# Performance work log

Measured on AMD Instinct MI355X. Metric: run time of the kernel, lower is better.

## Reference

```python
import jax, jax.numpy as jnp
import numpy as np

N_HEAD = 16
MASKED_BIAS = -10000.0


def setup_inputs() -> dict:
    key = jax.random.key(0)
    k1, k2, k3 = jax.random.split(key, 3)
    B, T, E = 2, 2048, 1024
    return {
        "stacked": jax.random.normal(k1, (B, T, E), dtype=jnp.float32),
        "w_attn": jax.random.normal(k2, (E, 3 * E), dtype=jnp.float32) * 0.02,
        "b_attn": jnp.zeros((3 * E,), dtype=jnp.float32),
        "w_proj": jax.random.normal(k3, (E, E), dtype=jnp.float32) * 0.02,
        "b_proj": jnp.zeros((E,), dtype=jnp.float32),
    }


def reference(stacked, w_attn, b_attn, w_proj, b_proj):
    B, T, E = stacked.shape
    nh = N_HEAD
    dh = E // nh
    # Conv1D (GPT-2): x @ W + b
    qkv = stacked @ w_attn + b_attn            # (B, T, 3E)
    q, k, v = jnp.split(qkv, 3, axis=-1)
    q = q.reshape(B, T, nh, dh).transpose(0, 2, 1, 3)  # (B, nh, T, dh)
    k = k.reshape(B, T, nh, dh).transpose(0, 2, 1, 3)
    v = v.reshape(B, T, nh, dh).transpose(0, 2, 1, 3)
    # scores = Q @ K^T / sqrt(dh)
    w = jnp.einsum("bhtd,bhsd->bhts", q, k) / jnp.sqrt(jnp.float32(dh))
    causal = jnp.tril(jnp.ones((T, T), dtype=bool))
    w = jnp.where(causal, w, jnp.float32(MASKED_BIAS))
    w = jax.nn.softmax(w, axis=-1)
    out = jnp.einsum("bhts,bhsd->bhtd", w, v)  # (B, nh, T, dh)
    out = out.transpose(0, 2, 1, 3).reshape(B, T, E)
    attn_z = out @ w_proj + b_proj
    return attn_z
```

## Files before the change

kernel.cpp:

```cpp
#include <hip/hip_runtime.h>
#include <hip/hip_bf16.h>

#define B_ 2
#define T_ 2048
#define E_ 1024
#define NH 16
#define M_ (B_*T_)
#define N3E 3072

typedef __attribute__((ext_vector_type(8))) short short8;
typedef __attribute__((ext_vector_type(4))) float f32x4;

__device__ __forceinline__ unsigned short f2bf(float f) {
  unsigned u = __builtin_bit_cast(unsigned, f);
  unsigned r = 0x7FFFu + ((u >> 16) & 1u);
  return (unsigned short)((u + r) >> 16);
}

__device__ __forceinline__ float bf2f(unsigned short s) {
  return __builtin_bit_cast(float, ((unsigned)s) << 16);
}

__device__ __forceinline__ unsigned cvtpk(float a, float b) {
  unsigned r;
  asm("v_cvt_pk_bf16_f32 %0, %1, %2" : "=v"(r) : "v"(a), "v"(b));
  return r;
}

__device__ __forceinline__ float exp2fast(float x) {
  float r;
  asm("v_exp_f32 %0, %1" : "=v"(r) : "v"(x));
  return r;
}

__device__ __forceinline__ void gload16(const void* g, void* l) {
  __builtin_amdgcn_global_load_lds(
      (const __attribute__((address_space(1))) unsigned int*)g,
      (__attribute__((address_space(3))) unsigned int*)l, 16, 0, 0);
}

__device__ __forceinline__ f32x4 mfma16(short8 a, short8 b, f32x4 c) {
  return __builtin_amdgcn_mfma_f32_16x16x32_bf16(a, b, c, 0, 0, 0);
}

__global__ __launch_bounds__(256) void prep_kernel(
    const float* __restrict__ stacked, const float* __restrict__ w_attn,
    const float* __restrict__ w_proj, unsigned short* __restrict__ Abf,
    unsigned short* __restrict__ WaT, unsigned short* __restrict__ WpT) {
  __shared__ float tile[32][33];
  const int bx = blockIdx.x;
  const int tid = threadIdx.x;
  if (bx < 2048) {
    int i = bx * 256 + tid;
    const float4* p = (const float4*)stacked + (size_t)i * 2;
    float4 a = p[0], b = p[1];
    short8 o;
    o[0] = (short)f2bf(a.x); o[1] = (short)f2bf(a.y);
    o[2] = (short)f2bf(a.z); o[3] = (short)f2bf(a.w);
    o[4] = (short)f2bf(b.x); o[5] = (short)f2bf(b.y);
    o[6] = (short)f2bf(b.z); o[7] = (short)f2bf(b.w);
    *(short8*)(Abf + (size_t)i * 8) = o;
    return;
  }
  const float* in;
  unsigned short* out;
  int R, C, c0, r0;
  if (bx < 5120) {
    int b = bx - 2048;
    in = w_attn; out = WaT; R = E_; C = N3E;
    c0 = (b % 96) * 32; r0 = (b / 96) * 32;
  } else {
    int b = bx - 5120;
    in = w_proj; out = WpT; R = E_; C = E_;
    c0 = (b % 32) * 32; r0 = (b / 32) * 32;
  }
  int tx = tid & 31, ty = tid >> 5;
#pragma unroll
  for (int i = 0; i < 4; i++) {
    int r = ty + i * 8;
    tile[r][tx] = in[(size_t)(r0 + r) * C + c0 + tx];
  }
  __syncthreads();
#pragma unroll
  for (int i = 0; i < 4; i++) {
    int r = ty + i * 8;
    out[(size_t)(c0 + r) * R + r0 + tx] = f2bf(tile[tx][r]);
  }
}

__global__ __launch_bounds__(256) void vtrans_kernel(
    const unsigned short* __restrict__ qkv, unsigned short* __restrict__ Vt) {
  const int s0 = blockIdx.x * 64;
  const int c0 = blockIdx.y * 64;
  const int b = blockIdx.z;
  __shared__ unsigned short t[64][72];
  const int tid = threadIdx.x;
  const size_t rs = 3 * E_;
  const unsigned short* src = qkv + (size_t)(b * T_) * rs + 2 * E_;
#pragma unroll
  for (int p = 0; p < 2; p++) {
    int idx = tid + p * 256;
    int r = idx >> 3, c = (idx & 7) * 8;
    *(short8*)&t[r][c] = *(const short8*)(src + (size_t)(s0 + r) * rs + c0 + c);
  }
  __syncthreads();
#pragma unroll
  for (int p = 0; p < 2; p++) {
    int idx = tid + p * 256;
    int dr = idx >> 3, sc = (idx & 7) * 8;
    short8 o;
#pragma unroll
    for (int j = 0; j < 8; j++) o[j] = (short)t[sc + j][dr];
    *(short8*)&Vt[(size_t)(b * E_ + c0 + dr) * T_ + s0 + sc] = o;
  }
}

__global__ __launch_bounds__(512, 2) void gemm256(
    const unsigned short* __restrict__ A, const unsigned short* __restrict__ Bt,
    const float* __restrict__ bias, unsigned short* __restrict__ outp,
    int M, int N, int K) {
  __shared__ __attribute__((aligned(16))) unsigned short Asm[2][256 * 64];
  __shared__ __attribute__((aligned(16))) unsigned short Bsm[2][256 * 64];
  const int tid = threadIdx.x;
  const int lane = tid & 63, wid = tid >> 6;
  const int wr = wid >> 2, wcn = wid & 3;
  const int li = lane & 15, g = lane >> 4;
  const int sw = li & 7;

  const int ntx = N >> 8;
  const int nwg = (M >> 8) * ntx;
  const int cpx = nwg >> 3;
  const int logical = (blockIdx.x & 7) * cpx + (blockIdx.x >> 3);
  const int bm = (logical / ntx) << 8;
  const int bn = (logical % ntx) << 8;

  f32x4 acc[8][4] = {};

#pragma unroll
  for (int p = 0; p < 4; p++) {
    int idx = tid + p * 512;
    int r = idx >> 3, ch = idx & 7;
    gload16(A + (size_t)(bm + r) * K + ((ch ^ (r & 7)) << 3),
            (char*)&Asm[0][0] + idx * 16);
  }
#pragma unroll
  for (int p = 0; p < 4; p++) {
    int idx = tid + p * 512;
    int r = idx >> 3, ch = idx & 7;
    gload16(Bt + (size_t)(bn + r) * K + ((ch ^ (r & 7)) << 3),
            (char*)&Bsm[0][0] + idx * 16);
  }
  asm volatile("s_waitcnt vmcnt(0)" ::: "memory");
  __syncthreads();

  const int NT = K >> 6;
  for (int t = 0; t < NT; t++) {
    const int buf = t & 1;
    const unsigned short* As = &Asm[buf][0];
    const unsigned short* Bs = &Bsm[buf][0];
    const int kn = (t + 1) << 6;
    const bool pre = (t + 1 < NT);
#pragma unroll
    for (int q = 0; q < 4; q++) {
      const int mh = q >> 1, nh2 = q & 1;
      short8 a[4][2], bfr[2][2];
#pragma unroll
      for (int mf = 0; mf < 4; mf++) {
        const int R = wr * 128 + (mh * 4 + mf) * 16 + li;
        a[mf][0] = *(const short8*)&As[R * 64 + ((g ^ sw) << 3)];
        a[mf][1] = *(const short8*)&As[R * 64 + (((4 + g) ^ sw) << 3)];
      }
#pragma unroll
      for (int nf = 0; nf < 2; nf++) {
        const int S = wcn * 64 + (nh2 * 2 + nf) * 16 + li;
        bfr[nf][0] = *(const short8*)&Bs[S * 64 + ((g ^ sw) << 3)];
        bfr[nf][1] = *(const short8*)&Bs[S * 64 + (((4 + g) ^ sw) << 3)];
      }
      if (pre && q == 0) {
#pragma unroll
        for (int p = 0; p < 4; p++) {
          int idx = tid + p * 512;
          int r = idx >> 3, ch = idx & 7;
          gload16(A + (size_t)(bm + r) * K + kn + ((ch ^ (r & 7)) << 3),
                  (char*)&Asm[buf ^ 1][0] + idx * 16);
        }
      }
      if (pre && q == 1) {
#pragma unroll
        for (int p = 0; p < 4; p++) {
          int idx = tid + p * 512;
          int r = idx >> 3, ch = idx & 7;
          gload16(Bt + (size_t)(bn + r) * K + kn + ((ch ^ (r & 7)) << 3),
                  (char*)&Bsm[buf ^ 1][0] + idx * 16);
        }
      }
      __builtin_amdgcn_sched_barrier(0);
      __builtin_amdgcn_s_setprio(1);
#pragma unroll
      for (int mf = 0; mf < 4; mf++)
#pragma unroll
        for (int nf = 0; nf < 2; nf++) {
          f32x4 c = acc[mh * 4 + mf][nh2 * 2 + nf];
          c = mfma16(a[mf][0], bfr[nf][0], c);
          c = mfma16(a[mf][1], bfr[nf][1], c);
          acc[mh * 4 + mf][nh2 * 2 + nf] = c;
        }
      __builtin_amdgcn_s_setprio(0);
      __builtin_amdgcn_sched_barrier(0);
    }
    asm volatile("s_waitcnt vmcnt(0)" ::: "memory");
    __syncthreads();
  }

#pragma unroll
  for (int nf = 0; nf < 4; nf++) {
    int col = bn + wcn * 64 + nf * 16 + li;
    float bs = bias[col];
#pragma unroll
    for (int mf = 0; mf < 8; mf++) {
      int row0 = bm + wr * 128 + mf * 16 + g * 4;
#pragma unroll
      for (int r = 0; r < 4; r++)
        outp[(size_t)(row0 + r) * N + col] = f2bf(acc[mf][nf][r] + bs);
    }
  }
}

template <int OUTF32>
__global__ __launch_bounds__(256) void gemm_bt(
    const unsigned short* __restrict__ A, const unsigned short* __restrict__ Bt,
    const float* __restrict__ bias, void* __restrict__ outp,
    int M, int N, int K) {
  __shared__ __attribute__((aligned(16))) unsigned short Asm[2][128 * 32];
  __shared__ __attribute__((aligned(16))) unsigned short Bsm[2][128 * 32];
  const int tid = threadIdx.x;
  const int lane = tid & 63;
  const int wid = tid >> 6;
  const int wr = wid >> 1, wc = wid & 1;
  const int li = lane & 15, g = lane >> 4;

  const int ntx = N >> 7;
  const int nwg = (M >> 7) * ntx;
  const int cpx = nwg >> 3;
  const int logical = (blockIdx.x & 7) * cpx + (blockIdx.x >> 3);
  const int bm = (logical / ntx) << 7;
  const int bn = (logical % ntx) << 7;

  f32x4 acc[4][4] = {};

  const int srow = tid >> 2;
  const int scol = (tid & 3) * 8;
  const unsigned short* Ag = A + (size_t)(bm + srow) * K + scol;
  const unsigned short* Bg = Bt + (size_t)(bn + srow) * K + scol;
  const int ldsoff = tid * 16;

  gload16(Ag, (char*)&Asm[0][0] + ldsoff);
  gload16(Ag + (size_t)64 * K, (char*)&Asm[0][0] + ldsoff + 4096);
  gload16(Bg, (char*)&Bsm[0][0] + ldsoff);
  gload16(Bg + (size_t)64 * K, (char*)&Bsm[0][0] + ldsoff + 4096);
  asm volatile("s_waitcnt vmcnt(0)" ::: "memory");
  __syncthreads();

  int cur = 0;
  for (int k0 = 0; k0 < K; k0 += 32) {
    const bool pre = (k0 + 32 < K);
    if (pre) {
      const int k1 = k0 + 32;
      gload16(Ag + k1, (char*)&Asm[cur ^ 1][0] + ldsoff);
      gload16(Ag + (size_t)64 * K + k1,
              (char*)&Asm[cur ^ 1][0] + ldsoff + 4096);
      gload16(Bg + k1, (char*)&Bsm[cur ^ 1][0] + ldsoff);
      gload16(Bg + (size_t)64 * K + k1,
              (char*)&Bsm[cur ^ 1][0] + ldsoff + 4096);
    }
    short8 af[4], bf[4];
#pragma unroll
    for (int i = 0; i < 4; i++)
      af[i] = *(const short8*)&Asm[cur][(wr * 64 + i * 16 + li) * 32 + g * 8];
#pragma unroll
    for (int j = 0; j < 4; j++)
      bf[j] = *(const short8*)&Bsm[cur][(wc * 64 + j * 16 + li) * 32 + g * 8];
    __builtin_amdgcn_s_setprio(1);
#pragma unroll
    for (int i = 0; i < 4; i++)
#pragma unroll
      for (int j = 0; j < 4; j++)
        acc[i][j] = __builtin_amdgcn_mfma_f32_16x16x32_bf16(af[i], bf[j],
                                                            acc[i][j], 0, 0, 0);
    __builtin_amdgcn_s_setprio(0);
    if (pre) asm volatile("s_waitcnt vmcnt(0)" ::: "memory");
    __syncthreads();
    cur ^= 1;
  }

#pragma unroll
  for (int j = 0; j < 4; j++) {
    int col = bn + wc * 64 + j * 16 + li;
    float bs = bias[col];
#pragma unroll
    for (int i = 0; i < 4; i++) {
      int row0 = bm + wr * 64 + i * 16 + g * 4;
#pragma unroll
      for (int r = 0; r < 4; r++) {
        float v = acc[i][j][r] + bs;
        if (OUTF32)
          ((float*)outp)[(size_t)(row0 + r) * N + col] = v;
        else
          ((unsigned short*)outp)[(size_t)(row0 + r) * N + col] = f2bf(v);
      }
    }
  }
}

__device__ __forceinline__ void attn_tile(
    const unsigned short* Ksm, const unsigned short* Vts,
    unsigned short (*PsmW)[64], short8 qf0, short8 qf1,
    float& m2, float& l2, f32x4* O, int qrel, bool diag, int li, int g) {
  f32x4 S[4];
  __builtin_amdgcn_s_setprio(1);
#pragma unroll
  for (int ct = 0; ct < 4; ct++) {
    int r = ct * 16 + li;
    int sw = r & 7;
    short8 k0f = *(const short8*)&Ksm[r * 64 + ((g ^ sw) << 3)];
    short8 k1f = *(const short8*)&Ksm[r * 64 + (((g + 4) ^ sw) << 3)];
    f32x4 z = {0.f, 0.f, 0.f, 0.f};
    z = mfma16(k0f, qf0, z);
    z = mfma16(k1f, qf1, z);
    S[ct] = z;
  }
  __builtin_amdgcn_s_setprio(0);

  if (diag) {
#pragma unroll
    for (int ct = 0; ct < 4; ct++)
#pragma unroll
      for (int r = 0; r < 4; r++)
        if (ct * 16 + g * 4 + r > qrel) S[ct][r] = -30000.f;
  }

  float tmax = S[0][0];
#pragma unroll
  for (int ct = 0; ct < 4; ct++)
#pragma unroll
    for (int r = 0; r < 4; r++) tmax = fmaxf(tmax, S[ct][r]);
  tmax = fmaxf(tmax, __shfl_xor(tmax, 16));
  tmax = fmaxf(tmax, __shfl_xor(tmax, 32));

  if (__any(tmax > m2 + 11.5f)) {
    float mn = fmaxf(m2, tmax);
    float cs = exp2fast(m2 - mn);
    l2 *= cs;
#pragma unroll
    for (int c2 = 0; c2 < 4; c2++)
#pragma unroll
      for (int r = 0; r < 4; r++) O[c2][r] *= cs;
    m2 = mn;
  }

  float rsum = 0.f;
#pragma unroll
  for (int ct = 0; ct < 4; ct++) {
    float p0 = exp2fast(S[ct][0] - m2);
    float p1 = exp2fast(S[ct][1] - m2);
    float p2 = exp2fast(S[ct][2] - m2);
    float p3 = exp2fast(S[ct][3] - m2);
    rsum += (p0 + p1) + (p2 + p3);
    uint2 pk;
    pk.x = cvtpk(p0, p1);
    pk.y = cvtpk(p2, p3);
    int pc = (2 * ct + (g >> 1)) ^ (li & 7);
    *(uint2*)&PsmW[li][pc * 8 + (g & 1) * 4] = pk;
  }
  rsum += __shfl_xor(rsum, 16);
  rsum += __shfl_xor(rsum, 32);
  l2 += rsum;

  __builtin_amdgcn_s_setprio(1);
#pragma unroll
  for (int kk = 0; kk < 2; kk++) {
    short8 pf = *(const short8*)&PsmW[li][((4 * kk + g) ^ (li & 7)) * 8];
#pragma unroll
    for (int c2 = 0; c2 < 4; c2++) {
      int d = c2 * 16 + li;
      short8 vf = *(const short8*)&Vts[d * 64 + (((kk * 4 + g) ^ (li & 7)) << 3)];
      O[c2] = mfma16(vf, pf, O[c2]);
    }
  }
  __builtin_amdgcn_s_setprio(0);
}

__global__ __launch_bounds__(256) void attn_kernel(
    const unsigned short* __restrict__ qkv, const unsigned short* __restrict__ Vt,
    unsigned short* __restrict__ aout) {
  const int pair = blockIdx.x;
  const int h = blockIdx.y, b = blockIdx.z;
  const int qa = pair, qb = (T_ / 64 - 1) - pair;
  const int tid = threadIdx.x, lane = tid & 63, w = tid >> 6;
  const int li = lane & 15, g = lane >> 4;

  __shared__ __attribute__((aligned(16))) unsigned short Ksm[2][64 * 64];
  __shared__ __attribute__((aligned(16))) unsigned short Vts[2][64 * 64];
  __shared__ __attribute__((aligned(16))) unsigned short Psm[4][16][64];

  const size_t rs = 3 * E_;
  const unsigned short* base = qkv + (size_t)b * T_ * rs + h * 64;
  const unsigned short* Kg = base + E_;
  const unsigned short* Vtg = Vt + (size_t)(b * E_ + h * 64) * T_;

  const float QSC = 0.18033688f;
  short8 qfa0, qfa1, qfb0, qfb1;
  {
    const unsigned short* qrow = base + (size_t)(qa * 64 + w * 16 + li) * rs;
    short8 v0 = *(const short8*)(qrow + g * 8);
    short8 v1 = *(const short8*)(qrow + 32 + g * 8);
    qrow = base + (size_t)(qb * 64 + w * 16 + li) * rs;
    short8 v2 = *(const short8*)(qrow + g * 8);
    short8 v3 = *(const short8*)(qrow + 32 + g * 8);
#pragma unroll
    for (int j = 0; j < 8; j++) {
      qfa0[j] = (short)f2bf(bf2f((unsigned short)v0[j]) * QSC);
      qfa1[j] = (short)f2bf(bf2f((unsigned short)v1[j]) * QSC);
      qfb0[j] = (short)f2bf(bf2f((unsigned short)v2[j]) * QSC);
      qfb1[j] = (short)f2bf(bf2f((unsigned short)v3[j]) * QSC);
    }
  }

  float ma = -1e30f, la = 0.f, mb = -1e30f, lb = 0.f;
  f32x4 Oa[4] = {}, Ob[4] = {};

#pragma unroll
  for (int p = 0; p < 2; p++) {
    int idx = tid + p * 256;
    int r = idx >> 3, ch = idx & 7;
    int sc = (ch ^ (r & 7)) * 8;
    gload16(Kg + (size_t)r * rs + sc, (char*)&Ksm[0][0] + idx * 16);
    gload16(Vtg + (size_t)r * T_ + sc, (char*)&Vts[0][0] + idx * 16);
  }
  asm volatile("s_waitcnt vmcnt(0)" ::: "memory");
  __syncthreads();

  const int nt = qb + 1;
  for (int kv = 0; kv < nt; kv++) {
    const int cur = kv & 1, nxt = cur ^ 1;
    const bool pre = (kv + 1 < nt);
    if (pre) {
      const int s1 = (kv + 1) * 64;
#pragma unroll
      for (int p = 0; p < 2; p++) {
        int idx = tid + p * 256;
        int r = idx >> 3, ch = idx & 7;
        int sc = (ch ^ (r & 7)) * 8;
        gload16(Kg + (size_t)(s1 + r) * rs + sc,
                (char*)&Ksm[nxt][0] + idx * 16);
        gload16(Vtg + (size_t)r * T_ + s1 + sc,
                (char*)&Vts[nxt][0] + idx * 16);
      }
    }

    attn_tile(&Ksm[cur][0], &Vts[cur][0], Psm[w], qfb0, qfb1, mb, lb, Ob,
              qb * 64 + w * 16 + li - kv * 64, kv == qb, li, g);
    if (kv <= qa)
      attn_tile(&Ksm[cur][0], &Vts[cur][0], Psm[w], qfa0, qfa1, ma, la, Oa,
                qa * 64 + w * 16 + li - kv * 64, kv == qa, li, g);

    asm volatile("s_waitcnt vmcnt(0)" ::: "memory");
    __syncthreads();
  }

  const float inva = 1.f / la, invb = 1.f / lb;
  const int rowa = b * T_ + qa * 64 + w * 16 + li;
  const int rowb = b * T_ + qb * 64 + w * 16 + li;
#pragma unroll
  for (int c2 = 0; c2 < 4; c2++) {
    uint2 oa, ob;
    oa.x = cvtpk(Oa[c2][0] * inva, Oa[c2][1] * inva);
    oa.y = cvtpk(Oa[c2][2] * inva, Oa[c2][3] * inva);
    ob.x = cvtpk(Ob[c2][0] * invb, Ob[c2][1] * invb);
    ob.y = cvtpk(Ob[c2][2] * invb, Ob[c2][3] * invb);
    *(uint2*)&aout[(size_t)rowa * E_ + h * 64 + c2 * 16 + g * 4] = oa;
    *(uint2*)&aout[(size_t)rowb * E_ + h * 64 + c2 * 16 + g * 4] = ob;
  }
}

extern "C" void kernel_launch(void* const* d_in, const int* in_sizes, int n_in,
                              void* d_out, int out_size, void* d_ws,
                              size_t ws_size, hipStream_t stream) {
  const float* stacked = (const float*)d_in[0];
  const float* w_attn = (const float*)d_in[1];
  const float* b_attn = (const float*)d_in[2];
  const float* w_proj = (const float*)d_in[3];
  const float* b_proj = (const float*)d_in[4];
  float* out = (float*)d_out;

  unsigned short* Abf = (unsigned short*)d_ws;
  unsigned short* WaT = Abf + (size_t)M_ * E_;
  unsigned short* WpT = WaT + (size_t)N3E * E_;
  unsigned short* qkv = WpT + (size_t)E_ * E_;
  unsigned short* aout = qkv + (size_t)M_ * N3E;
  unsigned short* Vt = aout + (size_t)M_ * E_;

  prep_kernel<<<6144, 256, 0, stream>>>(stacked, w_attn, w_proj, Abf, WaT, WpT);
  gemm256<<<(M_ / 256) * (N3E / 256), 512, 0, stream>>>(Abf, WaT, b_attn, qkv,
                                                        M_, N3E, E_);
  vtrans_kernel<<<dim3(T_ / 64, E_ / 64, B_), 256, 0, stream>>>(qkv, Vt);
  attn_kernel<<<dim3(T_ / 128, NH, B_), 256, 0, stream>>>(qkv, Vt, aout);
  gemm_bt<1><<<(M_ / 128) * (E_ / 128), 256, 0, stream>>>(aout, WpT, b_proj,
                                                          out, M_, E_, E_);
}
```

Measured before the change: 118.1 us.

## Fuse V transpose into QKV GEMM epilogue and retile to 256x192

```diff
diff --git a/kernel.cpp b/kernel.cpp
--- a/kernel.cpp
+++ b/kernel.cpp
@@ -88,53 +88,26 @@
   }
 }
 
-__global__ __launch_bounds__(256) void vtrans_kernel(
-    const unsigned short* __restrict__ qkv, unsigned short* __restrict__ Vt) {
-  const int s0 = blockIdx.x * 64;
-  const int c0 = blockIdx.y * 64;
-  const int b = blockIdx.z;
-  __shared__ unsigned short t[64][72];
-  const int tid = threadIdx.x;
-  const size_t rs = 3 * E_;
-  const unsigned short* src = qkv + (size_t)(b * T_) * rs + 2 * E_;
-#pragma unroll
-  for (int p = 0; p < 2; p++) {
-    int idx = tid + p * 256;
-    int r = idx >> 3, c = (idx & 7) * 8;
-    *(short8*)&t[r][c] = *(const short8*)(src + (size_t)(s0 + r) * rs + c0 + c);
-  }
-  __syncthreads();
-#pragma unroll
-  for (int p = 0; p < 2; p++) {
-    int idx = tid + p * 256;
-    int dr = idx >> 3, sc = (idx & 7) * 8;
-    short8 o;
-#pragma unroll
-    for (int j = 0; j < 8; j++) o[j] = (short)t[sc + j][dr];
-    *(short8*)&Vt[(size_t)(b * E_ + c0 + dr) * T_ + s0 + sc] = o;
-  }
-}
-
-__global__ __launch_bounds__(512, 2) void gemm256(
+__global__ __launch_bounds__(512, 1) void gemm256(
     const unsigned short* __restrict__ A, const unsigned short* __restrict__ Bt,
-    const float* __restrict__ bias, unsigned short* __restrict__ outp,
-    int M, int N, int K) {
+    const float* __restrict__ bias, unsigned short* __restrict__ qkvout,
+    unsigned short* __restrict__ Vt, int M, int N, int K) {
   __shared__ __attribute__((aligned(16))) unsigned short Asm[2][256 * 64];
-  __shared__ __attribute__((aligned(16))) unsigned short Bsm[2][256 * 64];
+  __shared__ __attribute__((aligned(16))) unsigned short Bsm[2][192 * 64];
   const int tid = threadIdx.x;
   const int lane = tid & 63, wid = tid >> 6;
   const int wr = wid >> 2, wcn = wid & 3;
   const int li = lane & 15, g = lane >> 4;
   const int sw = li & 7;
 
-  const int ntx = N >> 8;
+  const int ntx = N / 192;
   const int nwg = (M >> 8) * ntx;
   const int cpx = nwg >> 3;
   const int logical = (blockIdx.x & 7) * cpx + (blockIdx.x >> 3);
   const int bm = (logical / ntx) << 8;
-  const int bn = (logical % ntx) << 8;
-
-  f32x4 acc[8][4] = {};
+  const int bn = (logical % ntx) * 192;
+
+  f32x4 acc[8][3] = {};
 
 #pragma unroll
   for (int p = 0; p < 4; p++) {
@@ -144,7 +117,7 @@
             (char*)&Asm[0][0] + idx * 16);
   }
 #pragma unroll
-  for (int p = 0; p < 4; p++) {
+  for (int p = 0; p < 3; p++) {
     int idx = tid + p * 512;
     int r = idx >> 3, ch = idx & 7;
     gload16(Bt + (size_t)(bn + r) * K + ((ch ^ (r & 7)) << 3),
@@ -160,23 +133,22 @@
     const unsigned short* Bs = &Bsm[buf][0];
     const int kn = (t + 1) << 6;
     const bool pre = (t + 1 < NT);
-#pragma unroll
-    for (int q = 0; q < 4; q++) {
-      const int mh = q >> 1, nh2 = q & 1;
-      short8 a[4][2], bfr[2][2];
-#pragma unroll
-      for (int mf = 0; mf < 4; mf++) {
-        const int R = wr * 128 + (mh * 4 + mf) * 16 + li;
-        a[mf][0] = *(const short8*)&As[R * 64 + ((g ^ sw) << 3)];
-        a[mf][1] = *(const short8*)&As[R * 64 + (((4 + g) ^ sw) << 3)];
-      }
-#pragma unroll
-      for (int nf = 0; nf < 2; nf++) {
-        const int S = wcn * 64 + (nh2 * 2 + nf) * 16 + li;
-        bfr[nf][0] = *(const short8*)&Bs[S * 64 + ((g ^ sw) << 3)];
-        bfr[nf][1] = *(const short8*)&Bs[S * 64 + (((4 + g) ^ sw) << 3)];
-      }
-      if (pre && q == 0) {
+    short8 a[4][2];
+#pragma unroll
+    for (int ph = 0; ph < 6; ph++) {
+      const int mh = ph / 3, nf3 = ph % 3;
+      if (nf3 == 0) {
+#pragma unroll
+        for (int mf = 0; mf < 4; mf++) {
+          const int R = wr * 128 + (mh * 4 + mf) * 16 + li;
+          a[mf][0] = *(const short8*)&As[R * 64 + ((g ^ sw) << 3)];
+          a[mf][1] = *(const short8*)&As[R * 64 + (((4 + g) ^ sw) << 3)];
+        }
+      }
+      const int S = wcn * 48 + nf3 * 16 + li;
+      short8 b0 = *(const short8*)&Bs[S * 64 + ((g ^ sw) << 3)];
+      short8 b1 = *(const short8*)&Bs[S * 64 + (((4 + g) ^ sw) << 3)];
+      if (pre && ph == 0) {
 #pragma unroll
         for (int p = 0; p < 4; p++) {
           int idx = tid + p * 512;
@@ -185,9 +157,9 @@
                   (char*)&Asm[buf ^ 1][0] + idx * 16);
         }
       }
-      if (pre && q == 1) {
-#pragma unroll
-        for (int p = 0; p < 4; p++) {
+      if (pre && ph == 1) {
+#pragma unroll
+        for (int p = 0; p < 3; p++) {
           int idx = tid + p * 512;
           int r = idx >> 3, ch = idx & 7;
           gload16(Bt + (size_t)(bn + r) * K + kn + ((ch ^ (r & 7)) << 3),
@@ -197,14 +169,12 @@
       __builtin_amdgcn_sched_barrier(0);
       __builtin_amdgcn_s_setprio(1);
 #pragma unroll
-      for (int mf = 0; mf < 4; mf++)
-#pragma unroll
-        for (int nf = 0; nf < 2; nf++) {
-          f32x4 c = acc[mh * 4 + mf][nh2 * 2 + nf];
-          c = mfma16(a[mf][0], bfr[nf][0], c);
-          c = mfma16(a[mf][1], bfr[nf][1], c);
-          acc[mh * 4 + mf][nh2 * 2 + nf] = c;
-        }
+      for (int mf = 0; mf < 4; mf++) {
+        f32x4 c = acc[mh * 4 + mf][nf3];
+        c = mfma16(a[mf][0], b0, c);
+        c = mfma16(a[mf][1], b1, c);
+        acc[mh * 4 + mf][nf3] = c;
+      }
       __builtin_amdgcn_s_setprio(0);
       __builtin_amdgcn_sched_barrier(0);
     }
@@ -213,15 +183,28 @@
   }
 
 #pragma unroll
-  for (int nf = 0; nf < 4; nf++) {
-    int col = bn + wcn * 64 + nf * 16 + li;
+  for (int nf = 0; nf < 3; nf++) {
+    int col = bn + wcn * 48 + nf * 16 + li;
     float bs = bias[col];
-#pragma unroll
-    for (int mf = 0; mf < 8; mf++) {
-      int row0 = bm + wr * 128 + mf * 16 + g * 4;
-#pragma unroll
-      for (int r = 0; r < 4; r++)
-        outp[(size_t)(row0 + r) * N + col] = f2bf(acc[mf][nf][r] + bs);
+    if (col < 2 * E_) {
+#pragma unroll
+      for (int mf = 0; mf < 8; mf++) {
+        int row0 = bm + wr * 128 + mf * 16 + g * 4;
+#pragma unroll
+        for (int r = 0; r < 4; r++)
+          qkvout[(size_t)(row0 + r) * N + col] = f2bf(acc[mf][nf][r] + bs);
+      }
+    } else {
+      const int c = col - 2 * E_;
+#pragma unroll
+      for (int mf = 0; mf < 8; mf++) {
+        int row0 = bm + wr * 128 + mf * 16 + g * 4;
+        int bq = row0 >> 11, s0 = row0 & 2047;
+        uint2 o;
+        o.x = cvtpk(acc[mf][nf][0] + bs, acc[mf][nf][1] + bs);
+        o.y = cvtpk(acc[mf][nf][2] + bs, acc[mf][nf][3] + bs);
+        *(uint2*)&Vt[(size_t)(bq * E_ + c) * T_ + s0] = o;
+      }
     }
   }
 }
@@ -501,9 +484,8 @@
   unsigned short* Vt = aout + (size_t)M_ * E_;
 
   prep_kernel<<<6144, 256, 0, stream>>>(stacked, w_attn, w_proj, Abf, WaT, WpT);
-  gemm256<<<(M_ / 256) * (N3E / 256), 512, 0, stream>>>(Abf, WaT, b_attn, qkv,
-                                                        M_, N3E, E_);
-  vtrans_kernel<<<dim3(T_ / 64, E_ / 64, B_), 256, 0, stream>>>(qkv, Vt);
+  gemm256<<<(M_ / 256) * (N3E / 192), 512, 0, stream>>>(Abf, WaT, b_attn, qkv,
+                                                        Vt, M_, N3E, E_);
   attn_kernel<<<dim3(T_ / 128, NH, B_), 256, 0, stream>>>(qkv, Vt, aout);
   gemm_bt<1><<<(M_ / 128) * (E_ / 128), 256, 0, stream>>>(aout, WpT, b_proj,
                                                           out, M_, E_, E_);
```

Measured after the change: 114.5 us. 1.03x faster.
